# Performance work log

Hardware: AMD Instinct MI355X
Metric: run time of the kernel (lower is better)

Reference implementation:

```python
import jax, jax.numpy as jnp
import numpy as np
from jax import lax

B, M = 16384, 128
NUM_LAYERS, OW, OH = 22, 11, 11
MAX_VEC = np.array([9.0, 1.0, 1.0, 10.0, 3.0, 254.0, 1.0, 1.0, 235.0, 8.0, 9.0, 250.0,
                    29.0, 1.0, 1.0, 8.0, 1.0, 1.0, 6.0, 3.0, 1.0, 2.0], dtype=np.float32)


def setup_inputs() -> dict:
    key = jax.random.key(0)
    ks = jax.random.split(key, 20)
    s = 0.05
    return {
        "observations": jax.random.randint(ks[0], (B, M, 3), 0, 255, dtype=jnp.int32),
        "cnn1_w": jax.random.normal(ks[1], (64, 22, 5, 5), jnp.float32) * s,
        "cnn1_b": jnp.zeros((64,), jnp.float32),
        "cnn2_w": jax.random.normal(ks[2], (64, 64, 3, 3), jnp.float32) * s,
        "cnn2_b": jnp.zeros((64,), jnp.float32),
        "fc1_w": jax.random.normal(ks[3], (128, 64), jnp.float32) * s,
        "fc1_b": jnp.zeros((128,), jnp.float32),
        "enc_w": jax.random.normal(ks[4], (128, 128), jnp.float32) * s,
        "enc_b": jnp.zeros((128,), jnp.float32),
        "critic1_w": jax.random.normal(ks[5], (1024, 128), jnp.float32) * s,
        "critic1_b": jnp.zeros((1024,), jnp.float32),
        "value_w": jax.random.normal(ks[6], (1, 1024), jnp.float32) * s,
        "value_b": jnp.zeros((1,), jnp.float32),
        "actor1_w": jax.random.normal(ks[7], (512, 128), jnp.float32) * s,
        "actor1_b": jnp.zeros((512,), jnp.float32),
        "action_emb": jax.random.normal(ks[8], (100, 16), jnp.float32) * s,
        "head0_w": jax.random.normal(ks[9], (9, 528), jnp.float32) * s,
        "head0_b": jnp.zeros((9,), jnp.float32),
        "head1_w": jax.random.normal(ks[10], (10, 528), jnp.float32) * s,
        "head1_b": jnp.zeros((10,), jnp.float32),
    }


def _encode_scatter(observations):
    # zero-out any byte equal to 255 (matches torch in-place masking)
    tok = jnp.where(observations == 255, 0, observations)  # [B, M, 3]
    coords = tok[..., 0].astype(jnp.uint8)
    x = ((coords >> 4) & 15).astype(jnp.int32)
    y = (coords & 15).astype(jnp.int32)
    atr = tok[..., 1].astype(jnp.int32)
    val = tok[..., 2].astype(jnp.float32)
    b, m = atr.shape
    valid = (x < OW) & (y < OH) & (atr < NUM_LAYERS)
    b_idx = jnp.broadcast_to(jnp.arange(b, dtype=jnp.int32)[:, None], (b, m))
    b_idx = jnp.where(valid, b_idx, b)  # route invalid tokens out of bounds -> dropped
    box = jnp.zeros((b, NUM_LAYERS, OW, OH), jnp.float32)
    box = box.at[b_idx, atr, x, y].set(val, mode="drop")
    return box


def _forward(observations, cnn1_w, cnn1_b, cnn2_w, cnn2_b, fc1_w, fc1_b, enc_w, enc_b,
             critic1_w, critic1_b, value_w, value_b, actor1_w, actor1_b, action_emb,
             head0_w, head0_b, head1_w, head1_b):
    box = _encode_scatter(observations)
    x = box / jnp.asarray(MAX_VEC)[None, :, None, None]
    dn = ("NCHW", "OIHW", "NCHW")
    x = lax.conv_general_dilated(x, cnn1_w, (3, 3), "VALID", dimension_numbers=dn) + cnn1_b[None, :, None, None]
    x = lax.conv_general_dilated(x, cnn2_w, (1, 1), "VALID", dimension_numbers=dn) + cnn2_b[None, :, None, None]
    x = x.reshape(x.shape[0], -1)                 # [B, 64]
    x = x @ fc1_w.T + fc1_b                       # [B, 128]
    hidden = x @ enc_w.T + enc_b                  # [B, 128]
    critic = jnp.tanh(hidden @ critic1_w.T + critic1_b)
    value = critic @ value_w.T + value_b          # [B, 1]
    actor = hidden @ actor1_w.T + actor1_b        # [B, 512]
    emb = jnp.broadcast_to(action_emb.mean(axis=0)[None, :], (actor.shape[0], action_emb.shape[1]))
    comb = jnp.concatenate([actor, emb], axis=-1)  # [B, 528]
    logits = jnp.concatenate([comb @ head0_w.T + head0_b, comb @ head1_w.T + head1_b], axis=-1)
    return logits, value


def reference(observations, cnn1_w, cnn1_b, cnn2_w, cnn2_b, fc1_w, fc1_b, enc_w, enc_b,
              critic1_w, critic1_b, value_w, value_b, actor1_w, actor1_b, action_emb,
              head0_w, head0_b, head1_w, head1_b):
    return _forward(observations, cnn1_w, cnn1_b, cnn2_w, cnn2_b, fc1_w, fc1_b, enc_w, enc_b,
                    critic1_w, critic1_b, value_w, value_b, actor1_w, actor1_b, action_emb,
                    head0_w, head0_b, head1_w, head1_b)
```

## Files before the change

kernel.cpp:

```cpp
#include <hip/hip_runtime.h>
#include <math.h>

#define NB 16384
#define NTOK 128
#define NKEY 2662
#define NLOG 19
#define TB 8

typedef __attribute__((ext_vector_type(8))) short short8;
typedef __attribute__((ext_vector_type(4))) float floatx4;

struct Tok3 { int x, y, z; };

__device__ __constant__ float c_maxv[22] = {
    9.f, 1.f, 1.f, 10.f, 3.f, 254.f, 1.f, 1.f, 235.f, 8.f, 9.f, 250.f,
    29.f, 1.f, 1.f, 8.f, 1.f, 1.f, 6.f, 3.f, 1.f, 2.f};

__device__ __forceinline__ unsigned short f2bf(float f) {
    unsigned u = __float_as_uint(f);
    return (unsigned short)((u + 0x7FFFu + ((u >> 16) & 1u)) >> 16);
}
__device__ __forceinline__ float tanh_fast(float x) {
    float e = __builtin_amdgcn_exp2f(x * 2.885390082f);
    return 1.f - 2.f * __builtin_amdgcn_rcpf(e + 1.f);
}

__global__ __launch_bounds__(256) void k_preA(
    const float* __restrict__ w1, const float* __restrict__ b1,
    const float* __restrict__ w2, const float* __restrict__ b2,
    const float* __restrict__ fc1w, const float* __restrict__ fc1b,
    const float* __restrict__ encw, const float* __restrict__ encb,
    const float* __restrict__ a1w, const float* __restrict__ a1b,
    const float* __restrict__ aemb,
    const float* __restrict__ h0w, const float* __restrict__ h0b,
    const float* __restrict__ h1w, const float* __restrict__ h1b,
    const float* __restrict__ c1w,
    float* __restrict__ W2Ft, float* __restrict__ encwT,
    float* __restrict__ beff, float* __restrict__ blog,
    float* __restrict__ Wlog, unsigned short* __restrict__ c1wb)
{
    __shared__ float sF[64 * 129];
    const int bid = blockIdx.x, t = threadIdx.x;

    if (bid < 72) {
        #pragma unroll
        for (int r = 0; r < 32; ++r) {
            int idx = t + 256 * r;
            int p_ = idx >> 6, v_ = idx & 63;
            sF[v_ * 129 + p_] = fc1w[idx];
        }
        __syncthreads();
        #pragma unroll
        for (int r = 0; r < 4; ++r) {
            int idx = t + 256 * r;
            int p = idx & 127;
            int uk = __builtin_amdgcn_readfirstlane(bid * 8 + (idx >> 7));
            float acc = 0.f;
            #pragma unroll 8
            for (int v = 0; v < 64; ++v)
                acc += sF[v * 129 + p] * w2[v * 576 + uk];
            W2Ft[uk * 128 + p] = acc;
        }
    } else if (bid == 72) {
        float* s_part = sF;
        float* s_h2b  = sF + 256;
        float* s_t    = sF + 320;
        {
            int v = t & 63, part = t >> 6;
            float s = 0.f;
            for (int u = part * 16; u < part * 16 + 16; ++u) {
                float ws = 0.f;
                #pragma unroll
                for (int k = 0; k < 9; ++k) ws += w2[v * 576 + u * 9 + k];
                s += b1[u] * ws;
            }
            s_part[part * 64 + v] = s;
        }
        __syncthreads();
        if (t < 64)
            s_h2b[t] = b2[t] + s_part[t] + s_part[64 + t] + s_part[128 + t] + s_part[192 + t];
        __syncthreads();
        if (t < 128) {
            float s = fc1b[t];
            for (int v = 0; v < 64; ++v) s += fc1w[t * 64 + v] * s_h2b[v];
            s_t[t] = s;
        }
        __syncthreads();
        if (t < 128) {
            float s = encb[t];
            for (int p = 0; p < 128; ++p) s += encw[t * 128 + p] * s_t[p];
            beff[t] = s;
        }
    } else if (bid == 73) {
        float* s_cat = sF;
        float* s_p   = sF + 528;
        if (t < 16) {
            float s = 0.f;
            for (int r = 0; r < 100; ++r) s += aemb[r * 16 + t];
            s_cat[512 + t] = s * 0.01f;
        } else if (t >= 64 && t < 64 + 128) {
            s_cat[t - 64] = a1b[t - 64];
            s_cat[t - 64 + 128] = a1b[t - 64 + 128];
            s_cat[t - 64 + 256] = a1b[t - 64 + 256];
            s_cat[t - 64 + 384] = a1b[t - 64 + 384];
        }
        __syncthreads();
        if (t < 247) {
            int o = t / 13, ch = t % 13;
            const float* hw = (o < 9) ? (h0w + o * 528) : (h1w + (o - 9) * 528);
            int i0 = ch * 41, i1 = i0 + 41; if (i1 > 528) i1 = 528;
            float s = 0.f;
            for (int i = i0; i < i1; ++i) s += hw[i] * s_cat[i];
            s_p[t] = s;
        }
        __syncthreads();
        if (t < NLOG) {
            float s = (t < 9) ? h0b[t] : h1b[t - 9];
            #pragma unroll
            for (int ch = 0; ch < 13; ++ch) s += s_p[t * 13 + ch];
            blog[t] = s;
        }
    } else if (bid < 85) {
        int n = (bid - 74) * 256 + t;
        if (n < NLOG * 128) {
            int o = __builtin_amdgcn_readfirstlane(n >> 7);
            int h = n & 127;
            const float* hw = (o < 9) ? (h0w + o * 528) : (h1w + (o - 9) * 528);
            float acc = 0.f;
            #pragma unroll 8
            for (int a = 0; a < 512; ++a)
                acc += hw[a] * a1w[a * 128 + h];
            Wlog[n] = acc;
        }
    } else if (bid < 101) {
        #pragma unroll
        for (int r = 0; r < 32; ++r) {
            int n = (bid - 85) * 8192 + t + 256 * r;
            c1wb[n] = f2bf(c1w[n]);
        }
    } else {
        #pragma unroll
        for (int r = 0; r < 8; ++r) {
            int idx = (bid - 101) * 2048 + t + 256 * r;
            int h = idx >> 7, p = idx & 127;
            encwT[p * 128 + h] = encw[idx];
        }
    }
}

__global__ __launch_bounds__(256) void k_preB(
    const float* __restrict__ W2Ft, const float* __restrict__ w1,
    const float* __restrict__ encwT, float* __restrict__ Weff)
{
    __shared__ float s_pA[2][128];
    __shared__ float s_A[128];
    const int t = threadIdx.x, key = blockIdx.x;
    const int half = t >> 7, p = t & 127;
    const int c = key / 121, rem = key % 121, X = rem / 11, Y = rem % 11;

    float acc = 0.f;
    for (int u = half * 32; u < half * 32 + 32; ++u) {
        const float* w1u = w1 + u * 550 + c * 25;
        #pragma unroll
        for (int i = 0; i < 3; ++i) {
            int xi = X - 3 * i;
            if (xi < 0 || xi > 4) continue;
            #pragma unroll
            for (int j = 0; j < 3; ++j) {
                int yj = Y - 3 * j;
                if (yj < 0 || yj > 4) continue;
                acc += w1u[xi * 5 + yj] * W2Ft[(u * 9 + i * 3 + j) * 128 + p];
            }
        }
    }
    s_pA[half][p] = acc;
    __syncthreads();
    if (half == 0) s_A[p] = (s_pA[0][p] + s_pA[1][p]) / c_maxv[c];
    __syncthreads();

    float o = 0.f;
    #pragma unroll 8
    for (int p2 = half * 64; p2 < half * 64 + 64; ++p2)
        o += encwT[p2 * 128 + p] * s_A[p2];
    s_pA[half][p] = o;
    __syncthreads();
    if (t < 128) Weff[key * 128 + t] = s_pA[0][t] + s_pA[1][t];
}

__global__ __launch_bounds__(256) void k_hidden(
    const int* __restrict__ obs,
    const float* __restrict__ Weff, const float* __restrict__ beff,
    const float* __restrict__ Wlog, const float* __restrict__ blog,
    unsigned short* __restrict__ hb, float* __restrict__ out)
{
    __shared__ int   s_lst[TB * 32];
    __shared__ float s_hidden[TB * 128];
    __shared__ int   s_cnt[TB];

    const int tid = threadIdx.x, bid = blockIdx.x;
    const int b0 = bid * TB;

    if (tid < TB) s_cnt[tid] = 0;
    __syncthreads();

    {
        const Tok3* obs3 = (const Tok3*)obs;
        const int gtok0 = b0 * NTOK;
        #pragma unroll
        for (int k = 0; k < TB * NTOK / 256; ++k) {
            int tt = tid + 256 * k;
            Tok3 o = obs3[gtok0 + tt];
            int o0 = (o.x == 255) ? 0 : o.x;
            int o1 = (o.y == 255) ? 0 : o.y;
            int o2 = (o.z == 255) ? 0 : o.z;
            int x = (o0 >> 4) & 15, y = o0 & 15;
            if (x < 11 && y < 11 && o1 < 22) {
                int bb = tt >> 7, m = tt & 127;
                int pos = atomicAdd(&s_cnt[bb], 1);
                if (pos < 32)
                    s_lst[bb * 32 + pos] = (m << 20) | (o2 << 12) | (o1 * 121 + x * 11 + y);
            }
        }
    }
    __syncthreads();

    {
        int bb = tid >> 5, e = tid & 31;
        int n = s_cnt[bb]; if (n > 32) n = 32;
        if (e < n) {
            int p = s_lst[bb * 32 + e];
            bool dead = false;
            for (int i = 0; i < n; ++i) {
                int q = s_lst[bb * 32 + i];
                dead |= (((q ^ p) & 0xFFF) == 0) && (q > p);
            }
            if (dead) s_lst[bb * 32 + e] = p & ~0x000FF000;
        }
    }
    __syncthreads();

    {
        int h = tid & 127, bg = tid >> 7;
        for (int bb = bg; bb < TB; bb += 2) {
            float acc = beff[h];
            int n = s_cnt[bb]; if (n > 32) n = 32;
            for (int i = 0; i < n; ++i) {
                int p = s_lst[bb * 32 + i];
                acc += (float)((p >> 12) & 0xFF) * Weff[(p & 0xFFF) * 128 + h];
            }
            s_hidden[bb * 128 + h] = acc;
            hb[(b0 + bb) * 128 + h] = f2bf(acc);
        }
    }
    __syncthreads();

    {
        const float4* s_h4 = (const float4*)s_hidden;
        const float4* wl4  = (const float4*)Wlog;
        int bl = tid >> 5, o = tid & 31;
        if (o < NLOG) {
            float acc = blog[o];
            #pragma unroll
            for (int hq = 0; hq < 32; ++hq) {
                float4 hv = s_h4[bl * 32 + hq];
                float4 wl = wl4[o * 32 + hq];
                acc += wl.x * hv.x + wl.y * hv.y + wl.z * hv.z + wl.w * hv.w;
            }
            out[(b0 + bl) * NLOG + o] = acc;
        }
    }
}

__global__ __launch_bounds__(256) void k_gemm(
    const unsigned short* __restrict__ hb,
    const unsigned short* __restrict__ c1wb, const float* __restrict__ c1b,
    const float* __restrict__ vw, float* __restrict__ vpartial)
{
    __shared__ unsigned short sA[64 * 136];
    __shared__ float s_vp[4][64];

    const int tid = threadIdx.x, bid = blockIdx.x;
    const int nb = bid & 3;
    const int b0 = (bid >> 2) * 64;

    {
        const short8* hb8 = (const short8*)(hb + b0 * 128);
        #pragma unroll
        for (int i = 0; i < 4; ++i) {
            int idx = tid + 256 * i;
            int r = idx >> 4, c = idx & 15;
            *(short8*)&sA[r * 136 + c * 8] = hb8[idx];
        }
    }
    __syncthreads();

    const int lane = tid & 63, w = tid >> 6;
    const int lm = lane & 15, quad = lane >> 4;

    floatx4 acc[4][4];
    #pragma unroll
    for (int mt = 0; mt < 4; ++mt)
        #pragma unroll
        for (int nt = 0; nt < 4; ++nt)
            acc[mt][nt] = (floatx4){0.f, 0.f, 0.f, 0.f};

    #pragma unroll
    for (int ks = 0; ks < 4; ++ks) {
        short8 af[4];
        #pragma unroll
        for (int mt = 0; mt < 4; ++mt)
            af[mt] = *(const short8*)&sA[(mt * 16 + lm) * 136 + ks * 32 + quad * 8];
        #pragma unroll
        for (int nt = 0; nt < 4; ++nt) {
            int j = nb * 256 + w * 64 + nt * 16 + lm;
            short8 bf = *(const short8*)&c1wb[j * 128 + ks * 32 + quad * 8];
            #pragma unroll
            for (int mt = 0; mt < 4; ++mt)
                acc[mt][nt] = __builtin_amdgcn_mfma_f32_16x16x32_bf16(af[mt], bf, acc[mt][nt], 0, 0, 0);
        }
    }

    #pragma unroll
    for (int mt = 0; mt < 4; ++mt) {
        float vp[4] = {0.f, 0.f, 0.f, 0.f};
        #pragma unroll
        for (int nt = 0; nt < 4; ++nt) {
            int j = nb * 256 + w * 64 + nt * 16 + lm;
            float bj = c1b[j], wj = vw[j];
            #pragma unroll
            for (int r = 0; r < 4; ++r)
                vp[r] += tanh_fast(acc[mt][nt][r] + bj) * wj;
        }
        #pragma unroll
        for (int off = 1; off <= 8; off <<= 1)
            #pragma unroll
            for (int r = 0; r < 4; ++r)
                vp[r] += __shfl_xor(vp[r], off, 64);
        if (lm == 0) {
            #pragma unroll
            for (int r = 0; r < 4; ++r)
                s_vp[w][mt * 16 + quad * 4 + r] = vp[r];
        }
    }
    __syncthreads();
    if (tid < 64)
        vpartial[nb * NB + b0 + tid] =
            s_vp[0][tid] + s_vp[1][tid] + s_vp[2][tid] + s_vp[3][tid];
}

__global__ __launch_bounds__(256) void k_fin(
    const float* __restrict__ vpartial, const float* __restrict__ vb,
    float* __restrict__ out)
{
    int i = blockIdx.x * 256 + threadIdx.x;
    out[NB * NLOG + i] = vb[0] + vpartial[i] + vpartial[NB + i]
                       + vpartial[2 * NB + i] + vpartial[3 * NB + i];
}

extern "C" void kernel_launch(void* const* d_in, const int* in_sizes, int n_in,
                              void* d_out, int out_size, void* d_ws, size_t ws_size,
                              hipStream_t stream)
{
    const int*   obs  = (const int*)  d_in[0];
    const float* w1   = (const float*)d_in[1];
    const float* b1   = (const float*)d_in[2];
    const float* w2   = (const float*)d_in[3];
    const float* b2   = (const float*)d_in[4];
    const float* fc1w = (const float*)d_in[5];
    const float* fc1b = (const float*)d_in[6];
    const float* encw = (const float*)d_in[7];
    const float* encb = (const float*)d_in[8];
    const float* c1w  = (const float*)d_in[9];
    const float* c1b  = (const float*)d_in[10];
    const float* vw   = (const float*)d_in[11];
    const float* vb   = (const float*)d_in[12];
    const float* a1w  = (const float*)d_in[13];
    const float* a1b  = (const float*)d_in[14];
    const float* aemb = (const float*)d_in[15];
    const float* h0w  = (const float*)d_in[16];
    const float* h0b  = (const float*)d_in[17];
    const float* h1w  = (const float*)d_in[18];
    const float* h1b  = (const float*)d_in[19];

    float* W     = (float*)d_ws;
    float* W2Ft  = W;
    float* encwT = W + 73728;
    float* beff  = W + 90112;
    float* blog  = W + 90240;
    float* Wlog  = W + 90272;
    float* Weff  = W + 92704;
    unsigned short* c1wb = (unsigned short*)(W + 433440);
    unsigned short* hb   = (unsigned short*)(W + 498976);
    float* vpart = W + 1547552;

    hipLaunchKernelGGL(k_preA, dim3(109), dim3(256), 0, stream,
                       w1, b1, w2, b2, fc1w, fc1b, encw, encb, a1w, a1b, aemb,
                       h0w, h0b, h1w, h1b, c1w,
                       W2Ft, encwT, beff, blog, Wlog, c1wb);
    hipLaunchKernelGGL(k_preB, dim3(NKEY), dim3(256), 0, stream,
                       W2Ft, w1, encwT, Weff);
    hipLaunchKernelGGL(k_hidden, dim3(NB / TB), dim3(256), 0, stream,
                       obs, Weff, beff, Wlog, blog, hb, (float*)d_out);
    hipLaunchKernelGGL(k_gemm, dim3(1024), dim3(256), 0, stream,
                       hb, c1wb, c1b, vw, vpart);
    hipLaunchKernelGGL(k_fin, dim3(64), dim3(256), 0, stream,
                       vpart, vb, (float*)d_out);
}
```

Baseline: 211.8 us.

## Fuse hidden, critic GEMM and value reduction into one kernel

```diff
diff --git a/kernel.cpp b/kernel.cpp
--- a/kernel.cpp
+++ b/kernel.cpp
@@ -5,7 +5,7 @@
 #define NTOK 128
 #define NKEY 2662
 #define NLOG 19
-#define TB 8
+#define TB 64
 
 typedef __attribute__((ext_vector_type(8))) short short8;
 typedef __attribute__((ext_vector_type(4))) float floatx4;
@@ -187,15 +187,19 @@
     if (t < 128) Weff[key * 128 + t] = s_pA[0][t] + s_pA[1][t];
 }
 
-__global__ __launch_bounds__(256) void k_hidden(
+__global__ __launch_bounds__(256) void k_fused(
     const int* __restrict__ obs,
     const float* __restrict__ Weff, const float* __restrict__ beff,
+    const unsigned short* __restrict__ c1wb, const float* __restrict__ c1b,
+    const float* __restrict__ vw, const float* __restrict__ vb,
     const float* __restrict__ Wlog, const float* __restrict__ blog,
-    unsigned short* __restrict__ hb, float* __restrict__ out)
+    float* __restrict__ out)
 {
-    __shared__ int   s_lst[TB * 32];
-    __shared__ float s_hidden[TB * 128];
-    __shared__ int   s_cnt[TB];
+    __shared__ int            s_lst[TB * 32];
+    __shared__ float          s_hidden[TB * 128];
+    __shared__ unsigned short s_hb[TB * 136];
+    __shared__ int            s_cnt[TB];
+    __shared__ float          s_val[4][TB];
 
     const int tid = threadIdx.x, bid = blockIdx.x;
     const int b0 = bid * TB;
@@ -225,136 +229,116 @@
     __syncthreads();
 
     {
-        int bb = tid >> 5, e = tid & 31;
+        int bb = tid >> 2, e0 = tid & 3;
         int n = s_cnt[bb]; if (n > 32) n = 32;
-        if (e < n) {
-            int p = s_lst[bb * 32 + e];
-            bool dead = false;
-            for (int i = 0; i < n; ++i) {
-                int q = s_lst[bb * 32 + i];
-                dead |= (((q ^ p) & 0xFFF) == 0) && (q > p);
-            }
-            if (dead) s_lst[bb * 32 + e] = p & ~0x000FF000;
+        #pragma unroll
+        for (int r = 0; r < 8; ++r) {
+            int e = e0 + 4 * r;
+            if (e < n) {
+                int p = s_lst[bb * 32 + e];
+                bool dead = false;
+                for (int i = 0; i < n; ++i) {
+                    int q = s_lst[bb * 32 + i];
+                    dead |= (((q ^ p) & 0xFFF) == 0) && (q > p);
+                }
+                if (dead) s_lst[bb * 32 + e] = p & ~0x000FF000;
+            }
         }
     }
     __syncthreads();
 
     {
         int h = tid & 127, bg = tid >> 7;
+        float be = beff[h];
         for (int bb = bg; bb < TB; bb += 2) {
-            float acc = beff[h];
+            float acc = be;
             int n = s_cnt[bb]; if (n > 32) n = 32;
             for (int i = 0; i < n; ++i) {
                 int p = s_lst[bb * 32 + i];
                 acc += (float)((p >> 12) & 0xFF) * Weff[(p & 0xFFF) * 128 + h];
             }
             s_hidden[bb * 128 + h] = acc;
-            hb[(b0 + bb) * 128 + h] = f2bf(acc);
-        }
-    }
-    __syncthreads();
+            s_hb[bb * 136 + h] = f2bf(acc);
+        }
+    }
+    __syncthreads();
+
+    {
+        const int lane = tid & 63, w = tid >> 6;
+        const int lm = lane & 15, quad = lane >> 4;
+
+        short8 af[4][4];
+        #pragma unroll
+        for (int mt = 0; mt < 4; ++mt)
+            #pragma unroll
+            for (int ks = 0; ks < 4; ++ks)
+                af[mt][ks] = *(const short8*)&s_hb[(mt * 16 + lm) * 136 + ks * 32 + quad * 8];
+
+        float vp[4][4];
+        #pragma unroll
+        for (int mt = 0; mt < 4; ++mt)
+            #pragma unroll
+            for (int r = 0; r < 4; ++r) vp[mt][r] = 0.f;
+
+        for (int nt = 0; nt < 16; ++nt) {
+            int j = w * 256 + nt * 16 + lm;
+            short8 bf[4];
+            #pragma unroll
+            for (int ks = 0; ks < 4; ++ks)
+                bf[ks] = *(const short8*)&c1wb[j * 128 + ks * 32 + quad * 8];
+
+            #pragma unroll
+            for (int mt = 0; mt < 4; ++mt) {
+                floatx4 acc = {0.f, 0.f, 0.f, 0.f};
+                #pragma unroll
+                for (int ks = 0; ks < 4; ++ks)
+                    acc = __builtin_amdgcn_mfma_f32_16x16x32_bf16(af[mt][ks], bf[ks], acc, 0, 0, 0);
+                float bj = c1b[j], wj = vw[j];
+                #pragma unroll
+                for (int r = 0; r < 4; ++r)
+                    vp[mt][r] += tanh_fast(acc[r] + bj) * wj;
+            }
+        }
+        #pragma unroll
+        for (int off = 1; off <= 8; off <<= 1)
+            #pragma unroll
+            for (int mt = 0; mt < 4; ++mt)
+                #pragma unroll
+                for (int r = 0; r < 4; ++r)
+                    vp[mt][r] += __shfl_xor(vp[mt][r], off, 64);
+        if (lm == 0) {
+            #pragma unroll
+            for (int mt = 0; mt < 4; ++mt)
+                #pragma unroll
+                for (int r = 0; r < 4; ++r)
+                    s_val[w][mt * 16 + quad * 4 + r] = vp[mt][r];
+        }
+    }
+    __syncthreads();
+    if (tid < TB)
+        out[NB * NLOG + b0 + tid] = vb[0] +
+            s_val[0][tid] + s_val[1][tid] + s_val[2][tid] + s_val[3][tid];
 
     {
         const float4* s_h4 = (const float4*)s_hidden;
         const float4* wl4  = (const float4*)Wlog;
-        int bl = tid >> 5, o = tid & 31;
+        int bl0 = tid >> 5, o = tid & 31;
         if (o < NLOG) {
-            float acc = blog[o];
-            #pragma unroll
-            for (int hq = 0; hq < 32; ++hq) {
-                float4 hv = s_h4[bl * 32 + hq];
-                float4 wl = wl4[o * 32 + hq];
-                acc += wl.x * hv.x + wl.y * hv.y + wl.z * hv.z + wl.w * hv.w;
-            }
-            out[(b0 + bl) * NLOG + o] = acc;
-        }
-    }
-}
-
-__global__ __launch_bounds__(256) void k_gemm(
-    const unsigned short* __restrict__ hb,
-    const unsigned short* __restrict__ c1wb, const float* __restrict__ c1b,
-    const float* __restrict__ vw, float* __restrict__ vpartial)
-{
-    __shared__ unsigned short sA[64 * 136];
-    __shared__ float s_vp[4][64];
-
-    const int tid = threadIdx.x, bid = blockIdx.x;
-    const int nb = bid & 3;
-    const int b0 = (bid >> 2) * 64;
-
-    {
-        const short8* hb8 = (const short8*)(hb + b0 * 128);
-        #pragma unroll
-        for (int i = 0; i < 4; ++i) {
-            int idx = tid + 256 * i;
-            int r = idx >> 4, c = idx & 15;
-            *(short8*)&sA[r * 136 + c * 8] = hb8[idx];
-        }
-    }
-    __syncthreads();
-
-    const int lane = tid & 63, w = tid >> 6;
-    const int lm = lane & 15, quad = lane >> 4;
-
-    floatx4 acc[4][4];
-    #pragma unroll
-    for (int mt = 0; mt < 4; ++mt)
-        #pragma unroll
-        for (int nt = 0; nt < 4; ++nt)
-            acc[mt][nt] = (floatx4){0.f, 0.f, 0.f, 0.f};
-
-    #pragma unroll
-    for (int ks = 0; ks < 4; ++ks) {
-        short8 af[4];
-        #pragma unroll
-        for (int mt = 0; mt < 4; ++mt)
-            af[mt] = *(const short8*)&sA[(mt * 16 + lm) * 136 + ks * 32 + quad * 8];
-        #pragma unroll
-        for (int nt = 0; nt < 4; ++nt) {
-            int j = nb * 256 + w * 64 + nt * 16 + lm;
-            short8 bf = *(const short8*)&c1wb[j * 128 + ks * 32 + quad * 8];
-            #pragma unroll
-            for (int mt = 0; mt < 4; ++mt)
-                acc[mt][nt] = __builtin_amdgcn_mfma_f32_16x16x32_bf16(af[mt], bf, acc[mt][nt], 0, 0, 0);
-        }
-    }
-
-    #pragma unroll
-    for (int mt = 0; mt < 4; ++mt) {
-        float vp[4] = {0.f, 0.f, 0.f, 0.f};
-        #pragma unroll
-        for (int nt = 0; nt < 4; ++nt) {
-            int j = nb * 256 + w * 64 + nt * 16 + lm;
-            float bj = c1b[j], wj = vw[j];
-            #pragma unroll
-            for (int r = 0; r < 4; ++r)
-                vp[r] += tanh_fast(acc[mt][nt][r] + bj) * wj;
-        }
-        #pragma unroll
-        for (int off = 1; off <= 8; off <<= 1)
-            #pragma unroll
-            for (int r = 0; r < 4; ++r)
-                vp[r] += __shfl_xor(vp[r], off, 64);
-        if (lm == 0) {
-            #pragma unroll
-            for (int r = 0; r < 4; ++r)
-                s_vp[w][mt * 16 + quad * 4 + r] = vp[r];
-        }
-    }
-    __syncthreads();
-    if (tid < 64)
-        vpartial[nb * NB + b0 + tid] =
-            s_vp[0][tid] + s_vp[1][tid] + s_vp[2][tid] + s_vp[3][tid];
-}
-
-__global__ __launch_bounds__(256) void k_fin(
-    const float* __restrict__ vpartial, const float* __restrict__ vb,
-    float* __restrict__ out)
-{
-    int i = blockIdx.x * 256 + threadIdx.x;
-    out[NB * NLOG + i] = vb[0] + vpartial[i] + vpartial[NB + i]
-                       + vpartial[2 * NB + i] + vpartial[3 * NB + i];
+            float bo = blog[o];
+            #pragma unroll
+            for (int rep = 0; rep < 8; ++rep) {
+                int bl = bl0 + rep * 8;
+                float acc = bo;
+                #pragma unroll
+                for (int hq = 0; hq < 32; ++hq) {
+                    float4 hv = s_h4[bl * 32 + hq];
+                    float4 wl = wl4[o * 32 + hq];
+                    acc += wl.x * hv.x + wl.y * hv.y + wl.z * hv.z + wl.w * hv.w;
+                }
+                out[(b0 + bl) * NLOG + o] = acc;
+            }
+        }
+    }
 }
 
 extern "C" void kernel_launch(void* const* d_in, const int* in_sizes, int n_in,
@@ -390,8 +374,6 @@
     float* Wlog  = W + 90272;
     float* Weff  = W + 92704;
     unsigned short* c1wb = (unsigned short*)(W + 433440);
-    unsigned short* hb   = (unsigned short*)(W + 498976);
-    float* vpart = W + 1547552;
 
     hipLaunchKernelGGL(k_preA, dim3(109), dim3(256), 0, stream,
                        w1, b1, w2, b2, fc1w, fc1b, encw, encb, a1w, a1b, aemb,
@@ -399,10 +381,7 @@
                        W2Ft, encwT, beff, blog, Wlog, c1wb);
     hipLaunchKernelGGL(k_preB, dim3(NKEY), dim3(256), 0, stream,
                        W2Ft, w1, encwT, Weff);
-    hipLaunchKernelGGL(k_hidden, dim3(NB / TB), dim3(256), 0, stream,
-                       obs, Weff, beff, Wlog, blog, hb, (float*)d_out);
-    hipLaunchKernelGGL(k_gemm, dim3(1024), dim3(256), 0, stream,
-                       hb, c1wb, c1b, vw, vpart);
-    hipLaunchKernelGGL(k_fin, dim3(64), dim3(256), 0, stream,
-                       vpart, vb, (float*)d_out);
-}
+    hipLaunchKernelGGL(k_fused, dim3(NB / TB), dim3(256), 0, stream,
+                       obs, Weff, beff, c1wb, c1b, vw, vb, Wlog, blog,
+                       (float*)d_out);
+}
```

Measured after the change: 272.6 us. 28.7% more time.
